# Performance work log

Measured on AMD Instinct MI355X. Metric: run time of the kernel, lower is better.

The kernel has to match this reference:

```python
import jax, jax.numpy as jnp
import numpy as np

NB_HEAD = 4
SIZE_PER_HEAD = 50
D_MODEL = 200
B, S = 4, 4096


def setup_inputs() -> dict:
    key = jax.random.key(0)
    ks = jax.random.split(key, 7)
    q = jax.random.normal(ks[0], (B, S, D_MODEL), dtype=jnp.float32)
    k = jax.random.normal(ks[1], (B, S, D_MODEL), dtype=jnp.float32)
    v = jax.random.normal(ks[2], (B, S, D_MODEL), dtype=jnp.float32)
    # glorot-uniform-like init for weights
    def glorot(key, shape):
        lim = jnp.sqrt(6.0 / (shape[0] + shape[1])).astype(jnp.float32)
        return jax.random.uniform(key, shape, jnp.float32, -lim, lim)
    WQ = glorot(ks[3], (D_MODEL, SIZE_PER_HEAD))
    WK = glorot(ks[4], (D_MODEL, SIZE_PER_HEAD))
    WV = glorot(ks[5], (D_MODEL, SIZE_PER_HEAD))
    WO = glorot(ks[6], (NB_HEAD * SIZE_PER_HEAD, D_MODEL))
    return {"q": q, "k": k, "v": v, "WQ": WQ, "WK": WK, "WV": WV, "WO": WO}


def reference(q, k, v, WQ, WK, WV, WO):
    # The original per-head loop reuses the SAME WQ/WK/WV each iteration,
    # so every head output is identical. Compute attention once and tile.
    Qp = jnp.einsum('bsd,de->bse', q, WQ)  # [B,S,h]
    Kp = jnp.einsum('bsd,de->bse', k, WK)
    Vp = jnp.einsum('bsd,de->bse', v, WV)
    scale = 1.0 / jnp.sqrt(jnp.asarray(SIZE_PER_HEAD, dtype=Qp.dtype))
    A = jax.nn.softmax(jnp.einsum('bqe,bke->bqk', Qp, Kp) * scale, axis=-1)  # [B,S,S]
    O = jnp.einsum('bqk,bke->bqe', A, Vp)  # [B,S,h]
    O_concat = jnp.tile(O, (1, 1, NB_HEAD))  # [B,S,NB_HEAD*h]
    return jnp.einsum('bsf,fd->bsd', O_concat, WO)
```

## Files before the change

kernel.cpp:

```cpp
#include <hip/hip_runtime.h>
#include <hip/hip_bf16.h>


typedef short s4 __attribute__((ext_vector_type(4)));
typedef short s8 __attribute__((ext_vector_type(8)));
typedef float f4 __attribute__((ext_vector_type(4)));
typedef unsigned u2 __attribute__((ext_vector_type(2)));

#define SLEN 4096
#define NB 4
#define DMODEL 200
#define HREAL 50
#define HP 64
#define DMP 208
#define XPAD 212
#define KVB 64
#define QSCALE 0.20402789f
#define MFIX 24.0f

__device__ __forceinline__ short f2bf(float f) {
  unsigned u = __builtin_bit_cast(unsigned, f);
  u += 0x7FFFu + ((u >> 16) & 1u);
  return (short)(u >> 16);
}

__device__ __forceinline__ float bf2f(short s) {
  unsigned u = ((unsigned)(unsigned short)s) << 16;
  return __builtin_bit_cast(float, u);
}

__device__ __forceinline__ float fexp2(float x) { return __builtin_amdgcn_exp2f(x); }

__global__ __launch_bounds__(256) void proj_kernel(
    const float* __restrict__ q, const float* __restrict__ k, const float* __restrict__ v,
    const float* __restrict__ WQ, const float* __restrict__ WK, const float* __restrict__ WV,
    const float* __restrict__ WO, short* __restrict__ Qp, short* __restrict__ Kp,
    short* __restrict__ VpT, short* __restrict__ wot) {
  const int mode = blockIdx.z;
  const int tid = threadIdx.x;
  if (mode == 3) {
    int id = blockIdx.x * 256 + tid;
    if (blockIdx.x < 52 && id < DMP * HP) {
      int dm = id / HP, e = id % HP;
      float vv = 0.f;
      if (dm < DMODEL && e < HREAL) {
        vv = WO[(e)*DMODEL + dm] + WO[(HREAL + e) * DMODEL + dm] +
             WO[(2 * HREAL + e) * DMODEL + dm] + WO[(3 * HREAL + e) * DMODEL + dm];
      }
      wot[dm * HP + e] = f2bf(vv);
    }
    return;
  }
  __shared__ __align__(16) short Xl[64 * XPAD];
  __shared__ __align__(16) short Wl[64 * XPAD];
  const float* X = (mode == 0) ? q : (mode == 1 ? k : v);
  const float* Wsrc = (mode == 0) ? WQ : (mode == 1 ? WK : WV);
  const int sb64 = blockIdx.x * 64;

  {
    const f4* src = (const f4*)(X + (size_t)sb64 * DMODEL);
#pragma unroll
    for (int i = 0; i < 13; ++i) {
      int idx = tid + i * 256;
      if (idx < 3200) {
        f4 a = src[idx];
        int row = idx / 50, c = idx - row * 50;
        s4 bv;
#pragma unroll
        for (int j = 0; j < 4; ++j) bv[j] = f2bf(a[j]);
        *(s4*)(Xl + row * XPAD + c * 4) = bv;
      }
    }
    s4 z = {0, 0, 0, 0};
    if (tid < 192) {
      int row = tid / 3, c = 200 + (tid - (tid / 3) * 3) * 4;
      *(s4*)(Xl + row * XPAD + c) = z;
    }
#pragma unroll
    for (int i = 0; i < 40; ++i) {
      int flat = tid + i * 256;
      if (flat < DMODEL * HREAL) {
        float vv = Wsrc[flat];
        int d = flat / HREAL, e = flat - HREAL * d;
        if (mode == 0) vv *= QSCALE;
        Wl[e * XPAD + d] = f2bf(vv);
      }
    }
#pragma unroll
    for (int i = 0; i < 3; ++i) {
      int idx = tid + i * 256;
      if (idx < 742) *(s4*)(Wl + 50 * XPAD + idx * 4) = z;
    }
    if (tid < 150) {
      int row = tid / 3, c = 200 + (tid - (tid / 3) * 3) * 4;
      *(s4*)(Wl + row * XPAD + c) = z;
    }
  }
  __syncthreads();

  const int lane = tid & 63, wid = tid >> 6;
  const int l15 = lane & 15, g = lane >> 4;
  const int row16 = wid * 16 + l15;
  const int sbase = sb64 + wid * 16;
  f4 acc[4] = {};
#pragma unroll
  for (int c = 0; c < 13; ++c) {
    int d0 = 16 * c + 4 * g;
    s4 af = *(const s4*)(Xl + row16 * XPAD + d0);
#pragma unroll
    for (int n = 0; n < 4; ++n) {
      s4 bf = *(const s4*)(Wl + (16 * n + l15) * XPAD + d0);
      acc[n] = __builtin_amdgcn_mfma_f32_16x16x16bf16_1k(af, bf, acc[n], 0, 0, 0);
    }
  }
  if (mode < 2) {
    short* OUT = (mode == 0) ? Qp : Kp;
#pragma unroll
    for (int n = 0; n < 4; ++n)
#pragma unroll
      for (int r = 0; r < 4; ++r) {
        int rr = sbase + 4 * g + r;
        OUT[rr * HP + 16 * n + l15] = f2bf(acc[n][r]);
      }
  } else {
#pragma unroll
    for (int n = 0; n < 4; ++n)
#pragma unroll
      for (int r = 0; r < 4; ++r) {
        int rr = sbase + 4 * g + r;
        int bb = rr >> 12, s = rr & 4095;
        VpT[((bb * HP) + 16 * n + l15) * SLEN + s] = f2bf(acc[n][r]);
      }
  }
}

__global__ __launch_bounds__(256, 4) void attn_kernel(
    const short* __restrict__ Qp, const short* __restrict__ Kp,
    const short* __restrict__ VpT, float* __restrict__ Lp,
    short* __restrict__ Opb) {
  __shared__ __align__(16) char Klds[2][KVB * 128];
  __shared__ __align__(16) char Vlds[2][HP * 128];
  const int tid = threadIdx.x;
  const int lane = tid & 63, wid = tid >> 6;
  const int l15 = lane & 15, g = lane >> 4;
  const int b = blockIdx.y, z = blockIdx.z;
  const int nsplit = gridDim.z;
  const int qrowA = blockIdx.x * 128 + wid * 32 + l15;
  const int qrowB = qrowA + 16;
  const int ksw = (l15 & 7) << 4;

  s8 qfA[2], qfB[2];
  {
    const short* qpa = Qp + (size_t)(b * SLEN + qrowA) * HP + 8 * g;
    const short* qpb = Qp + (size_t)(b * SLEN + qrowB) * HP + 8 * g;
    qfA[0] = *(const s8*)(qpa);
    qfA[1] = *(const s8*)(qpa + 32);
    qfB[0] = *(const s8*)(qpb);
    qfB[1] = *(const s8*)(qpb + 32);
  }

  const int kr0 = l15 * 128 + ((16 * g) ^ ksw);
  const int kr1 = l15 * 128 + ((64 + 16 * g) ^ ksw);
  const int vb = l15 * 128 + ((8 * g) ^ ksw);

  const int cj0 = tid, cj1 = tid + 256;
  const int ci0 = (cj0 ^ ((cj0 >> 3) & 7)) * 16;
  const int ci1 = (cj1 ^ ((cj1 >> 3) & 7)) * 16;
  const int d0 = cj0 >> 3, d1 = cj1 >> 3;
  const int ch0 = ((cj0 & 7) ^ (d0 & 7)) * 16;
  const int ch1 = ((cj1 & 7) ^ (d1 & 7)) * 16;

  const int kv0 = z * (SLEN / nsplit);
  const char* kp0 = (const char*)Kp + (size_t)(b * SLEN + kv0) * 128 + ci0;
  const char* kp1 = (const char*)Kp + (size_t)(b * SLEN + kv0) * 128 + ci1;
  const char* vp0 =
      (const char*)VpT + ((size_t)(b * HP + d0) * SLEN + kv0) * 2 + ch0;
  const char* vp1 =
      (const char*)VpT + ((size_t)(b * HP + d1) * SLEN + kv0) * 2 + ch1;

  {
    f4 k0 = *(const f4*)kp0;
    f4 k1 = *(const f4*)kp1;
    f4 v0 = *(const f4*)vp0;
    f4 v1 = *(const f4*)vp1;
    *(f4*)(Klds[0] + tid * 16) = k0;
    *(f4*)(Klds[0] + tid * 16 + 4096) = k1;
    *(f4*)(Vlds[0] + tid * 16) = v0;
    *(f4*)(Vlds[0] + tid * 16 + 4096) = v1;
    kp0 += KVB * 128;
    kp1 += KVB * 128;
    vp0 += KVB * 2;
    vp1 += KVB * 2;
  }

  f4 oA[4] = {}, oB[4] = {};
  float lsumA = 0.f, lsumB = 0.f;
  const int nsteps = SLEN / nsplit / KVB;
  for (int step = 0; step < nsteps; ++step) {
    const int p = step & 1;
    f4 rk0, rk1, rv0, rv1;
    const bool more = (step + 1 < nsteps);
    if (more) {
      rk0 = *(const f4*)kp0;
      rk1 = *(const f4*)kp1;
      rv0 = *(const f4*)vp0;
      rv1 = *(const f4*)vp1;
      kp0 += KVB * 128;
      kp1 += KVB * 128;
      vp0 += KVB * 2;
      vp1 += KVB * 2;
    }
    __syncthreads();
    const char* Kbuf = Klds[p];
    const char* Vbuf = Vlds[p];
#pragma unroll
    for (int tt = 0; tt < 4; ++tt) {
      f4 stA, stB;
      {
        s8 kf0 = *(const s8*)(Kbuf + kr0 + tt * 2048);
        s8 kf1 = *(const s8*)(Kbuf + kr1 + tt * 2048);
        __builtin_amdgcn_s_setprio(1);
        stA = __builtin_amdgcn_mfma_f32_16x16x32_bf16(kf0, qfA[0], (f4){}, 0, 0, 0);
        stB = __builtin_amdgcn_mfma_f32_16x16x32_bf16(kf0, qfB[0], (f4){}, 0, 0, 0);
        stA = __builtin_amdgcn_mfma_f32_16x16x32_bf16(kf1, qfA[1], stA, 0, 0, 0);
        stB = __builtin_amdgcn_mfma_f32_16x16x32_bf16(kf1, qfB[1], stB, 0, 0, 0);
        __builtin_amdgcn_s_setprio(0);
      }
      float pa0 = fexp2(stA[0] - MFIX), pa1 = fexp2(stA[1] - MFIX);
      float pa2 = fexp2(stA[2] - MFIX), pa3 = fexp2(stA[3] - MFIX);
      lsumA += (pa0 + pa1) + (pa2 + pa3);
      union { unsigned u[2]; s4 s; } puA;
      asm("v_cvt_pk_bf16_f32 %0, %1, %2" : "=v"(puA.u[0]) : "v"(pa0), "v"(pa1));
      asm("v_cvt_pk_bf16_f32 %0, %1, %2" : "=v"(puA.u[1]) : "v"(pa2), "v"(pa3));
      s4 pfA = puA.s;
      float pb0 = fexp2(stB[0] - MFIX), pb1 = fexp2(stB[1] - MFIX);
      float pb2 = fexp2(stB[2] - MFIX), pb3 = fexp2(stB[3] - MFIX);
      lsumB += (pb0 + pb1) + (pb2 + pb3);
      union { unsigned u[2]; s4 s; } puB;
      asm("v_cvt_pk_bf16_f32 %0, %1, %2" : "=v"(puB.u[0]) : "v"(pb0), "v"(pb1));
      asm("v_cvt_pk_bf16_f32 %0, %1, %2" : "=v"(puB.u[1]) : "v"(pb2), "v"(pb3));
      s4 pfB = puB.s;
      const char* vrow = Vbuf + (vb ^ (tt << 5));
      __builtin_amdgcn_s_setprio(1);
#pragma unroll
      for (int n = 0; n < 4; ++n) {
        s4 vf = *(const s4*)(vrow + n * 2048);
        oA[n] = __builtin_amdgcn_mfma_f32_16x16x16bf16_1k(vf, pfA, oA[n], 0, 0, 0);
        oB[n] = __builtin_amdgcn_mfma_f32_16x16x16bf16_1k(vf, pfB, oB[n], 0, 0, 0);
      }
      __builtin_amdgcn_s_setprio(0);
    }
    if (more) {
      *(f4*)(Klds[p ^ 1] + tid * 16) = rk0;
      *(f4*)(Klds[p ^ 1] + tid * 16 + 4096) = rk1;
      *(f4*)(Vlds[p ^ 1] + tid * 16) = rv0;
      *(f4*)(Vlds[p ^ 1] + tid * 16 + 4096) = rv1;
    }
  }
  lsumA += __shfl_xor(lsumA, 16);
  lsumA += __shfl_xor(lsumA, 32);
  lsumB += __shfl_xor(lsumB, 16);
  lsumB += __shfl_xor(lsumB, 32);
  const int rowgA = b * SLEN + qrowA;
  const int rowgB = b * SLEN + qrowB;
  const int NR = NB * SLEN;
  if (lane < 16) {
    Lp[z * NR + rowgA] = lsumA;
    Lp[z * NR + rowgB] = lsumB;
  }
  short* opA = Opb + ((size_t)z * NR + rowgA) * HP;
  short* opB = Opb + ((size_t)z * NR + rowgB) * HP;
#pragma unroll
  for (int n = 0; n < 4; ++n) {
    u2 ua, ub;
    asm("v_cvt_pk_bf16_f32 %0, %1, %2" : "=v"(ua[0]) : "v"(oA[n][0]), "v"(oA[n][1]));
    asm("v_cvt_pk_bf16_f32 %0, %1, %2" : "=v"(ua[1]) : "v"(oA[n][2]), "v"(oA[n][3]));
    asm("v_cvt_pk_bf16_f32 %0, %1, %2" : "=v"(ub[0]) : "v"(oB[n][0]), "v"(oB[n][1]));
    asm("v_cvt_pk_bf16_f32 %0, %1, %2" : "=v"(ub[1]) : "v"(oB[n][2]), "v"(oB[n][3]));
    *(u2*)(opA + 16 * n + 4 * g) = ua;
    *(u2*)(opB + 16 * n + 4 * g) = ub;
  }
}

template <int NSPLIT>
__global__ __launch_bounds__(256) void combineproj_kernel(
    const float* __restrict__ Lp, const short* __restrict__ Opb,
    const short* __restrict__ wot, float* __restrict__ out) {
  const int lane = threadIdx.x & 63, wid = threadIdx.x >> 6;
  const int l15 = lane & 15, g = lane >> 4;
  const int sbase = blockIdx.x * 64 + wid * 16;
  const int row = sbase + l15;
  const int NR = NB * SLEN;
  float L = 0.f;
#pragma unroll
  for (int s = 0; s < NSPLIT; ++s) L += Lp[s * NR + row];
  float inv = 1.0f / L;
  s4 af[4];
#pragma unroll
  for (int c = 0; c < 4; ++c) {
    f4 acc = {};
#pragma unroll
    for (int s = 0; s < NSPLIT; ++s) {
      s4 sv = *(const s4*)(Opb + ((size_t)s * NR + row) * HP + 16 * c + 4 * g);
      acc[0] += bf2f(sv[0]);
      acc[1] += bf2f(sv[1]);
      acc[2] += bf2f(sv[2]);
      acc[3] += bf2f(sv[3]);
    }
#pragma unroll
    for (int r = 0; r < 4; ++r) af[c][r] = f2bf(acc[r] * inv);
  }
  for (int n = 0; n < 13; ++n) {
    f4 acc = {};
    const short* brow = wot + (16 * n + l15) * HP + 4 * g;
#pragma unroll
    for (int c = 0; c < 4; ++c) {
      s4 bf = *(const s4*)(brow + 16 * c);
      acc = __builtin_amdgcn_mfma_f32_16x16x16bf16_1k(af[c], bf, acc, 0, 0, 0);
    }
    int dm = 16 * n + l15;
    if (dm < DMODEL) {
#pragma unroll
      for (int r = 0; r < 4; ++r) {
        int rr = sbase + 4 * g + r;
        out[(size_t)rr * DMODEL + dm] = acc[r];
      }
    }
  }
}

extern "C" void kernel_launch(void* const* d_in, const int* in_sizes, int n_in,
                              void* d_out, int out_size, void* d_ws, size_t ws_size,
                              hipStream_t stream) {
  const float* q = (const float*)d_in[0];
  const float* k = (const float*)d_in[1];
  const float* v = (const float*)d_in[2];
  const float* WQ = (const float*)d_in[3];
  const float* WK = (const float*)d_in[4];
  const float* WV = (const float*)d_in[5];
  const float* WO = (const float*)d_in[6];
  float* out = (float*)d_out;
  char* ws = (char*)d_ws;

  const size_t MB2 = 2097152;
  const size_t NR = (size_t)NB * SLEN;
  auto need = [&](int n) {
    return (size_t)131072 + 3 * MB2 + (size_t)n * NR * 4 + (size_t)n * NR * HP * 2;
  };
  int nsplit = (ws_size >= need(8)) ? 8 : 4;

  short* wot = (short*)(ws + 98304);
  short* Qp = (short*)(ws + 131072);
  short* Kp = (short*)(ws + 131072 + MB2);
  short* VpT = (short*)(ws + 131072 + 2 * MB2);
  float* Lp = (float*)(ws + 131072 + 3 * MB2);
  short* Opb = (short*)(Lp + nsplit * NR);

  proj_kernel<<<dim3(256, 1, 4), dim3(256), 0, stream>>>(q, k, v, WQ, WK, WV, WO,
                                                          Qp, Kp, VpT, wot);
  attn_kernel<<<dim3(32, NB, nsplit), dim3(256), 0, stream>>>(Qp, Kp, VpT, Lp, Opb);
  if (nsplit == 8)
    combineproj_kernel<8><<<dim3(256), dim3(256), 0, stream>>>(Lp, Opb, wot, out);
  else
    combineproj_kernel<4><<<dim3(256), dim3(256), 0, stream>>>(Lp, Opb, wot, out);
}
```

Before: 62.03 us.

## Load K/V fragments directly from global memory instead of staging through LDS

Removes the double-buffered LDS staging of K and V tiles in the attention kernel, along with the per-step __syncthreads. Each wave now reads its MFMA operand fragments straight from global memory (via L1/L2) in 16-key steps, with unroll 2. The aim is to drop barrier and LDS traffic overhead, but the four waves now load the same K/V data redundantly. The global loads are narrow and strided (especially the 8-byte V fragments spread across SLEN-strided rows), so memory latency is exposed without explicit prefetch.

```diff
diff --git a/kernel.cpp b/kernel.cpp
--- a/kernel.cpp
+++ b/kernel.cpp
@@ -14,7 +14,6 @@
 #define HP 64
 #define DMP 208
 #define XPAD 212
-#define KVB 64
 #define QSCALE 0.20402789f
 #define MFIX 24.0f
 
@@ -138,8 +137,6 @@
     const short* __restrict__ Qp, const short* __restrict__ Kp,
     const short* __restrict__ VpT, float* __restrict__ Lp,
     short* __restrict__ Opb) {
-  __shared__ __align__(16) char Klds[2][KVB * 128];
-  __shared__ __align__(16) char Vlds[2][HP * 128];
   const int tid = threadIdx.x;
   const int lane = tid & 63, wid = tid >> 6;
   const int l15 = lane & 15, g = lane >> 4;
@@ -147,7 +144,6 @@
   const int nsplit = gridDim.z;
   const int qrowA = blockIdx.x * 128 + wid * 32 + l15;
   const int qrowB = qrowA + 16;
-  const int ksw = (l15 & 7) << 4;
 
   s8 qfA[2], qfB[2];
   {
@@ -159,103 +155,50 @@
     qfB[1] = *(const s8*)(qpb + 32);
   }
 
-  const int kr0 = l15 * 128 + ((16 * g) ^ ksw);
-  const int kr1 = l15 * 128 + ((64 + 16 * g) ^ ksw);
-  const int vb = l15 * 128 + ((8 * g) ^ ksw);
-
-  const int cj0 = tid, cj1 = tid + 256;
-  const int ci0 = (cj0 ^ ((cj0 >> 3) & 7)) * 16;
-  const int ci1 = (cj1 ^ ((cj1 >> 3) & 7)) * 16;
-  const int d0 = cj0 >> 3, d1 = cj1 >> 3;
-  const int ch0 = ((cj0 & 7) ^ (d0 & 7)) * 16;
-  const int ch1 = ((cj1 & 7) ^ (d1 & 7)) * 16;
-
   const int kv0 = z * (SLEN / nsplit);
-  const char* kp0 = (const char*)Kp + (size_t)(b * SLEN + kv0) * 128 + ci0;
-  const char* kp1 = (const char*)Kp + (size_t)(b * SLEN + kv0) * 128 + ci1;
-  const char* vp0 =
-      (const char*)VpT + ((size_t)(b * HP + d0) * SLEN + kv0) * 2 + ch0;
-  const char* vp1 =
-      (const char*)VpT + ((size_t)(b * HP + d1) * SLEN + kv0) * 2 + ch1;
-
-  {
-    f4 k0 = *(const f4*)kp0;
-    f4 k1 = *(const f4*)kp1;
-    f4 v0 = *(const f4*)vp0;
-    f4 v1 = *(const f4*)vp1;
-    *(f4*)(Klds[0] + tid * 16) = k0;
-    *(f4*)(Klds[0] + tid * 16 + 4096) = k1;
-    *(f4*)(Vlds[0] + tid * 16) = v0;
-    *(f4*)(Vlds[0] + tid * 16 + 4096) = v1;
-    kp0 += KVB * 128;
-    kp1 += KVB * 128;
-    vp0 += KVB * 2;
-    vp1 += KVB * 2;
-  }
+  const short* kbase = Kp + ((size_t)(b * SLEN + kv0 + l15)) * HP + 8 * g;
+  const short* vbase = VpT + ((size_t)(b * HP + l15)) * SLEN + kv0 + 4 * g;
 
   f4 oA[4] = {}, oB[4] = {};
   float lsumA = 0.f, lsumB = 0.f;
-  const int nsteps = SLEN / nsplit / KVB;
-  for (int step = 0; step < nsteps; ++step) {
-    const int p = step & 1;
-    f4 rk0, rk1, rv0, rv1;
-    const bool more = (step + 1 < nsteps);
-    if (more) {
-      rk0 = *(const f4*)kp0;
-      rk1 = *(const f4*)kp1;
-      rv0 = *(const f4*)vp0;
-      rv1 = *(const f4*)vp1;
-      kp0 += KVB * 128;
-      kp1 += KVB * 128;
-      vp0 += KVB * 2;
-      vp1 += KVB * 2;
-    }
-    __syncthreads();
-    const char* Kbuf = Klds[p];
-    const char* Vbuf = Vlds[p];
-#pragma unroll
-    for (int tt = 0; tt < 4; ++tt) {
-      f4 stA, stB;
-      {
-        s8 kf0 = *(const s8*)(Kbuf + kr0 + tt * 2048);
-        s8 kf1 = *(const s8*)(Kbuf + kr1 + tt * 2048);
-        __builtin_amdgcn_s_setprio(1);
-        stA = __builtin_amdgcn_mfma_f32_16x16x32_bf16(kf0, qfA[0], (f4){}, 0, 0, 0);
-        stB = __builtin_amdgcn_mfma_f32_16x16x32_bf16(kf0, qfB[0], (f4){}, 0, 0, 0);
-        stA = __builtin_amdgcn_mfma_f32_16x16x32_bf16(kf1, qfA[1], stA, 0, 0, 0);
-        stB = __builtin_amdgcn_mfma_f32_16x16x32_bf16(kf1, qfB[1], stB, 0, 0, 0);
-        __builtin_amdgcn_s_setprio(0);
-      }
-      float pa0 = fexp2(stA[0] - MFIX), pa1 = fexp2(stA[1] - MFIX);
-      float pa2 = fexp2(stA[2] - MFIX), pa3 = fexp2(stA[3] - MFIX);
-      lsumA += (pa0 + pa1) + (pa2 + pa3);
-      union { unsigned u[2]; s4 s; } puA;
-      asm("v_cvt_pk_bf16_f32 %0, %1, %2" : "=v"(puA.u[0]) : "v"(pa0), "v"(pa1));
-      asm("v_cvt_pk_bf16_f32 %0, %1, %2" : "=v"(puA.u[1]) : "v"(pa2), "v"(pa3));
-      s4 pfA = puA.s;
-      float pb0 = fexp2(stB[0] - MFIX), pb1 = fexp2(stB[1] - MFIX);
-      float pb2 = fexp2(stB[2] - MFIX), pb3 = fexp2(stB[3] - MFIX);
-      lsumB += (pb0 + pb1) + (pb2 + pb3);
-      union { unsigned u[2]; s4 s; } puB;
-      asm("v_cvt_pk_bf16_f32 %0, %1, %2" : "=v"(puB.u[0]) : "v"(pb0), "v"(pb1));
-      asm("v_cvt_pk_bf16_f32 %0, %1, %2" : "=v"(puB.u[1]) : "v"(pb2), "v"(pb3));
-      s4 pfB = puB.s;
-      const char* vrow = Vbuf + (vb ^ (tt << 5));
+  const int nt = SLEN / nsplit / 16;
+#pragma unroll 2
+  for (int t = 0; t < nt; ++t) {
+    f4 stA, stB;
+    {
+      const short* kp = kbase + (size_t)t * 16 * HP;
+      s8 kf0 = *(const s8*)(kp);
+      s8 kf1 = *(const s8*)(kp + 32);
       __builtin_amdgcn_s_setprio(1);
-#pragma unroll
-      for (int n = 0; n < 4; ++n) {
-        s4 vf = *(const s4*)(vrow + n * 2048);
-        oA[n] = __builtin_amdgcn_mfma_f32_16x16x16bf16_1k(vf, pfA, oA[n], 0, 0, 0);
-        oB[n] = __builtin_amdgcn_mfma_f32_16x16x16bf16_1k(vf, pfB, oB[n], 0, 0, 0);
-      }
+      stA = __builtin_amdgcn_mfma_f32_16x16x32_bf16(kf0, qfA[0], (f4){}, 0, 0, 0);
+      stB = __builtin_amdgcn_mfma_f32_16x16x32_bf16(kf0, qfB[0], (f4){}, 0, 0, 0);
+      stA = __builtin_amdgcn_mfma_f32_16x16x32_bf16(kf1, qfA[1], stA, 0, 0, 0);
+      stB = __builtin_amdgcn_mfma_f32_16x16x32_bf16(kf1, qfB[1], stB, 0, 0, 0);
       __builtin_amdgcn_s_setprio(0);
     }
-    if (more) {
-      *(f4*)(Klds[p ^ 1] + tid * 16) = rk0;
-      *(f4*)(Klds[p ^ 1] + tid * 16 + 4096) = rk1;
-      *(f4*)(Vlds[p ^ 1] + tid * 16) = rv0;
-      *(f4*)(Vlds[p ^ 1] + tid * 16 + 4096) = rv1;
-    }
+    float pa0 = fexp2(stA[0] - MFIX), pa1 = fexp2(stA[1] - MFIX);
+    float pa2 = fexp2(stA[2] - MFIX), pa3 = fexp2(stA[3] - MFIX);
+    lsumA += (pa0 + pa1) + (pa2 + pa3);
+    union { unsigned u[2]; s4 s; } puA;
+    asm("v_cvt_pk_bf16_f32 %0, %1, %2" : "=v"(puA.u[0]) : "v"(pa0), "v"(pa1));
+    asm("v_cvt_pk_bf16_f32 %0, %1, %2" : "=v"(puA.u[1]) : "v"(pa2), "v"(pa3));
+    s4 pfA = puA.s;
+    float pb0 = fexp2(stB[0] - MFIX), pb1 = fexp2(stB[1] - MFIX);
+    float pb2 = fexp2(stB[2] - MFIX), pb3 = fexp2(stB[3] - MFIX);
+    lsumB += (pb0 + pb1) + (pb2 + pb3);
+    union { unsigned u[2]; s4 s; } puB;
+    asm("v_cvt_pk_bf16_f32 %0, %1, %2" : "=v"(puB.u[0]) : "v"(pb0), "v"(pb1));
+    asm("v_cvt_pk_bf16_f32 %0, %1, %2" : "=v"(puB.u[1]) : "v"(pb2), "v"(pb3));
+    s4 pfB = puB.s;
+    const short* vp = vbase + 16 * t;
+    __builtin_amdgcn_s_setprio(1);
+#pragma unroll
+    for (int n = 0; n < 4; ++n) {
+      s4 vf = *(const s4*)(vp + (size_t)n * 16 * SLEN);
+      oA[n] = __builtin_amdgcn_mfma_f32_16x16x16bf16_1k(vf, pfA, oA[n], 0, 0, 0);
+      oB[n] = __builtin_amdgcn_mfma_f32_16x16x16bf16_1k(vf, pfB, oB[n], 0, 0, 0);
+    }
+    __builtin_amdgcn_s_setprio(0);
   }
   lsumA += __shfl_xor(lsumA, 16);
   lsumA += __shfl_xor(lsumA, 32);
```

After: 127.6 us. +105.7%, slower.
